# Performance work log

Measured on AMD Instinct MI355X. Metric: run time of the kernel, lower is better.

The kernel has to match this reference:

```python
import jax, jax.numpy as jnp
import numpy as np

NUM_ITER = 10  # torch forward default num_iter=10


def _normalize_rows(x):
    # x / (||x||_2 per row + 1e-6), matching torch data.norm(dim=1)[:, None]
    return x / (jnp.linalg.norm(x, axis=1, keepdims=True) + 1e-6)


def _cluster(data, init, cluster_temp, num_iter):
    # Soft k-means: normalize data once, then iterate
    # mu-normalize -> cosine sim -> softmax assignments -> weighted mean update.
    data = _normalize_rows(data)           # [N, D]
    mu = init                              # [K, D]
    dist = None
    for _ in range(num_iter):
        mu_n = _normalize_rows(mu)         # [K, D]
        dist = data @ mu_n.T               # [N, K]
        r = jax.nn.softmax(cluster_temp * dist, axis=1)  # [N, K]
        # diag(1/r.sum(0)) @ (r.T @ data) == row-wise divide
        mu = (r.T @ data) / r.sum(axis=0)[:, None]       # [K, D]
    r = jax.nn.softmax(cluster_temp * dist, axis=1)
    return mu, r


def setup_inputs() -> dict:
    key = jax.random.key(0)
    k1, k2 = jax.random.split(key)
    N, D, K = 100000, 512, 256
    embeds = jax.random.normal(k1, (N, D), dtype=jnp.float32)
    # self.init = torch.rand(K, nout): uniform [0, 1)
    init = jax.random.uniform(k2, (K, D), dtype=jnp.float32)
    cluster_temp = jnp.float32(30.0)
    return {"embeds": embeds, "cluster_temp": cluster_temp, "init": init}


def reference(embeds, cluster_temp, init):
    # First pass: 10 iterations from random init; result is detached in torch.
    mu_init, _ = _cluster(embeds, init, cluster_temp, NUM_ITER)
    mu_init = jax.lax.stop_gradient(mu_init)
    # Second pass: single iteration from detached means (grad flows here).
    mu, r = _cluster(embeds, mu_init, cluster_temp, 1)
    return mu, r
```

## Files before the change

### kernel.cpp

```cpp
#include <hip/hip_runtime.h>
#include <math.h>


#define DIMD 512
#define KCL 256
#define NSPLIT 96

typedef __attribute__((ext_vector_type(8))) short short8;
typedef __attribute__((ext_vector_type(4))) short short4v;
typedef __attribute__((ext_vector_type(4))) float float4v;

__device__ __forceinline__ short f2bf(float x) {
  union { float f; unsigned u; } v; v.f = x;
  unsigned r = v.u + 0x7fff + ((v.u >> 16) & 1);
  return (short)(r >> 16);
}
__device__ __forceinline__ float bf2f(short b) {
  union { unsigned u; float f; } v;
  v.u = ((unsigned)(unsigned short)b) << 16;
  return v.f;
}

__global__ void row_norms_k(const float* __restrict__ x,
                            float* __restrict__ inv_norm, int n) {
  int wave = threadIdx.x >> 6;
  int lane = threadIdx.x & 63;
  int row = blockIdx.x * 4 + wave;
  if (row >= n) return;
  const float4* xr = (const float4*)(x + (size_t)row * DIMD);
  float4 a = xr[lane];
  float4 b = xr[lane + 64];
  float s = a.x*a.x + a.y*a.y + a.z*a.z + a.w*a.w
          + b.x*b.x + b.y*b.y + b.z*b.z + b.w*b.w;
#pragma unroll
  for (int m = 32; m >= 1; m >>= 1) s += __shfl_xor(s, m);
  if (lane == 0) inv_norm[row] = 1.0f / (sqrtf(s) + 1e-6f);
}

__global__ void mu_norm_k(const float* __restrict__ mu_src,
                          const float* __restrict__ colsum_in,
                          short* __restrict__ mu_hi, short* __restrict__ mu_lo,
                          float* __restrict__ mu_acc_z,
                          float* __restrict__ colsum_z, int use_colsum) {
  int k = blockIdx.x;
  int t = threadIdx.x;
  float inv_c = 1.0f;
  if (use_colsum) inv_c = 1.0f / colsum_in[k];
  float v0 = mu_src[k * DIMD + t] * inv_c;
  float v1 = mu_src[k * DIMD + t + 256] * inv_c;
  float s = v0 * v0 + v1 * v1;
#pragma unroll
  for (int m = 32; m >= 1; m >>= 1) s += __shfl_xor(s, m);
  __shared__ float sred[4];
  int lane = t & 63, wv = t >> 6;
  if (lane == 0) sred[wv] = s;
  __syncthreads();
  s = sred[0] + sred[1] + sred[2] + sred[3];
  float inv = 1.0f / (sqrtf(s) + 1e-6f);
  float w0 = v0 * inv, w1 = v1 * inv;
  short h0 = f2bf(w0), h1 = f2bf(w1);
  mu_hi[k * DIMD + t] = h0;
  mu_hi[k * DIMD + t + 256] = h1;
  mu_lo[k * DIMD + t] = f2bf(w0 - bf2f(h0));
  mu_lo[k * DIMD + t + 256] = f2bf(w1 - bf2f(h1));
  mu_acc_z[k * DIMD + t] = 0.0f;
  mu_acc_z[k * DIMD + t + 256] = 0.0f;
  if (t == 0) colsum_z[k] = 0.0f;
}

__global__ void final_mu_k(const float* __restrict__ mu_acc,
                           const float* __restrict__ colsum,
                           float* __restrict__ out) {
  int k = blockIdx.x;
  int t = threadIdx.x;
  float ic = 1.0f / colsum[k];
  out[k * DIMD + t] = mu_acc[k * DIMD + t] * ic;
  out[k * DIMD + t + 256] = mu_acc[k * DIMD + t + 256] * ic;
}

__global__ __launch_bounds__(256) void dist_mfma_k(
    const float* __restrict__ data, const float* __restrict__ inv_norm,
    const short* __restrict__ mu_hi, const short* __restrict__ mu_lo,
    unsigned* __restrict__ r_pack, float* __restrict__ r_f32, int write_f32,
    float* __restrict__ colsum, const float* __restrict__ temp_p, int n) {
  __shared__ __align__(16) short a_lds[64][72];
  __shared__ __align__(16) short b_lds[256][72];
  __shared__ __align__(16) float red[64][4];

  int t = threadIdx.x;
  int wave = t >> 6, lane = t & 63, q = lane >> 4, lx = lane & 15;
  int i0 = blockIdx.x * 64;

  float4v acc[4][4];
#pragma unroll
  for (int mt = 0; mt < 4; ++mt)
#pragma unroll
    for (int nt = 0; nt < 4; ++nt) acc[mt][nt] = (float4v)0.0f;

  for (int ch = 0; ch < 16; ++ch) {
    int d0 = ch * 32;
    {
      int row = t >> 2, seg = t & 3;
      int gi = i0 + row;
      if (gi > n - 1) gi = n - 1;
      const float* p = data + (size_t)gi * DIMD + d0 + seg * 8;
      float4 x0 = *(const float4*)p;
      float4 x1 = *(const float4*)(p + 4);
      float sc = inv_norm[gi];
      float vv[8] = {x0.x * sc, x0.y * sc, x0.z * sc, x0.w * sc,
                     x1.x * sc, x1.y * sc, x1.z * sc, x1.w * sc};
      short8 hv, lv;
#pragma unroll
      for (int j = 0; j < 8; ++j) {
        short h = f2bf(vv[j]);
        hv[j] = h;
        lv[j] = f2bf(vv[j] - bf2f(h));
      }
      *(short8*)&a_lds[row][seg * 8] = hv;
      *(short8*)&a_lds[row][32 + seg * 8] = lv;
    }
    {
      int seg = t & 3, kb = t >> 2;
#pragma unroll
      for (int rep = 0; rep < 4; ++rep) {
        int k = rep * 64 + kb;
        short8 h = *(const short8*)(mu_hi + (size_t)k * DIMD + d0 + seg * 8);
        short8 l = *(const short8*)(mu_lo + (size_t)k * DIMD + d0 + seg * 8);
        *(short8*)&b_lds[k][seg * 8] = h;
        *(short8*)&b_lds[k][32 + seg * 8] = l;
      }
    }
    __syncthreads();
    short8 ah[4], al[4], bh[4], bl[4];
#pragma unroll
    for (int mt = 0; mt < 4; ++mt) {
      ah[mt] = *(const short8*)&a_lds[mt * 16 + lx][q * 8];
      al[mt] = *(const short8*)&a_lds[mt * 16 + lx][32 + q * 8];
    }
#pragma unroll
    for (int nt = 0; nt < 4; ++nt) {
      int kr = wave * 64 + nt * 16 + lx;
      bh[nt] = *(const short8*)&b_lds[kr][q * 8];
      bl[nt] = *(const short8*)&b_lds[kr][32 + q * 8];
    }
#pragma unroll
    for (int mt = 0; mt < 4; ++mt)
#pragma unroll
      for (int nt = 0; nt < 4; ++nt) {
        acc[mt][nt] = __builtin_amdgcn_mfma_f32_16x16x32_bf16(
            ah[mt], bh[nt], acc[mt][nt], 0, 0, 0);
        acc[mt][nt] = __builtin_amdgcn_mfma_f32_16x16x32_bf16(
            ah[mt], bl[nt], acc[mt][nt], 0, 0, 0);
        acc[mt][nt] = __builtin_amdgcn_mfma_f32_16x16x32_bf16(
            al[mt], bh[nt], acc[mt][nt], 0, 0, 0);
      }
    __syncthreads();
  }

  float tempv = temp_p[0];
  float rs[4][4];
#pragma unroll
  for (int mt = 0; mt < 4; ++mt)
#pragma unroll
    for (int reg = 0; reg < 4; ++reg) {
      float s = 0.0f;
#pragma unroll
      for (int nt = 0; nt < 4; ++nt) {
        float e = __expf(tempv * acc[mt][nt][reg]);
        acc[mt][nt][reg] = e;
        s += e;
      }
      s += __shfl_xor(s, 1);
      s += __shfl_xor(s, 2);
      s += __shfl_xor(s, 4);
      s += __shfl_xor(s, 8);
      rs[mt][reg] = s;
    }
  if (lx == 0) {
#pragma unroll
    for (int mt = 0; mt < 4; ++mt)
#pragma unroll
      for (int reg = 0; reg < 4; ++reg)
        red[mt * 16 + q * 4 + reg][wave] = rs[mt][reg];
  }
  __syncthreads();

  float cs[4] = {0.0f, 0.0f, 0.0f, 0.0f};
#pragma unroll
  for (int mt = 0; mt < 4; ++mt)
#pragma unroll
    for (int reg = 0; reg < 4; ++reg) {
      int row = mt * 16 + q * 4 + reg;
      float4 v = *(const float4*)&red[row][0];
      float is = 1.0f / (v.x + v.y + v.z + v.w);
      int gi = i0 + row;
      bool ok = gi < n;
#pragma unroll
      for (int nt = 0; nt < 4; ++nt) {
        float r = acc[mt][nt][reg] * is;
        acc[mt][nt][reg] = r;
        if (ok) cs[nt] += r;
      }
      if (ok) {
        if (write_f32) {
#pragma unroll
          for (int nt = 0; nt < 4; ++nt)
            r_f32[(size_t)gi * KCL + wave * 64 + nt * 16 + lx] =
                acc[mt][nt][reg];
        } else {
#pragma unroll
          for (int nt = 0; nt < 4; ++nt) {
            float r = acc[mt][nt][reg];
            short h = f2bf(r);
            short l = f2bf(r - bf2f(h));
            r_pack[(size_t)gi * KCL + wave * 64 + nt * 16 + lx] =
                ((unsigned)(unsigned short)h << 16) | (unsigned short)l;
          }
        }
      }
    }
#pragma unroll
  for (int nt = 0; nt < 4; ++nt) {
    cs[nt] += __shfl_xor(cs[nt], 16);
    cs[nt] += __shfl_xor(cs[nt], 32);
  }
  if (q == 0) {
#pragma unroll
    for (int nt = 0; nt < 4; ++nt)
      atomicAdd(&colsum[wave * 64 + nt * 16 + lx], cs[nt]);
  }
}

__global__ __launch_bounds__(256) void update_mfma_k(
    const unsigned* __restrict__ r_src, int r_is_f32,
    const float* __restrict__ data, const float* __restrict__ inv_norm,
    float* __restrict__ mu_acc, int n) {
  __shared__ __align__(16) short rT[128][72];
  __shared__ __align__(16) short xT[128][72];

  int t = threadIdx.x, wave = t >> 6, lane = t & 63, q = lane >> 4,
      lx = lane & 15;
  int bx = blockIdx.x;
  int k0 = (bx & 1) * 128, d0 = (bx >> 1) * 128;
  int ns = blockIdx.y;
  int chunk = (n + NSPLIT - 1) / NSPLIT;
  int ibeg = ns * chunk;
  int iend = ibeg + chunk;
  if (iend > n) iend = n;
  int wk = wave >> 1, wd = wave & 1;
  int iq = t >> 5, kq = t & 31;

  float4v acc[4][4];
#pragma unroll
  for (int mt = 0; mt < 4; ++mt)
#pragma unroll
    for (int nt = 0; nt < 4; ++nt) acc[mt][nt] = (float4v)0.0f;

  for (int ib = ibeg; ib < iend; ib += 32) {
    {
      short h[4][4], l[4][4];
#pragma unroll
      for (int ii = 0; ii < 4; ++ii) {
        int gi = ib + iq * 4 + ii;
        uint4 u = make_uint4(0u, 0u, 0u, 0u);
        if (gi < iend)
          u = *(const uint4*)(r_src + (size_t)gi * KCL + k0 + kq * 4);
        unsigned uu[4] = {u.x, u.y, u.z, u.w};
        if (r_is_f32) {
#pragma unroll
          for (int kk = 0; kk < 4; ++kk) {
            union { unsigned u; float f; } c; c.u = uu[kk];
            short hh = f2bf(c.f);
            h[ii][kk] = hh;
            l[ii][kk] = f2bf(c.f - bf2f(hh));
          }
        } else {
#pragma unroll
          for (int kk = 0; kk < 4; ++kk) {
            h[ii][kk] = (short)(uu[kk] >> 16);
            l[ii][kk] = (short)(uu[kk] & 0xffffu);
          }
        }
      }
#pragma unroll
      for (int kk = 0; kk < 4; ++kk) {
        short4v vh = {h[0][kk], h[1][kk], h[2][kk], h[3][kk]};
        short4v vl = {l[0][kk], l[1][kk], l[2][kk], l[3][kk]};
        *(short4v*)&rT[kq * 4 + kk][iq * 4] = vh;
        *(short4v*)&rT[kq * 4 + kk][32 + iq * 4] = vl;
      }
    }
    {
      short h[4][4], l[4][4];
#pragma unroll
      for (int ii = 0; ii < 4; ++ii) {
        int gi = ib + iq * 4 + ii;
        float4 x = make_float4(0.f, 0.f, 0.f, 0.f);
        float sc = 0.0f;
        if (gi < iend) {
          x = *(const float4*)(data + (size_t)gi * DIMD + d0 + kq * 4);
          sc = inv_norm[gi];
        }
        float vv[4] = {x.x * sc, x.y * sc, x.z * sc, x.w * sc};
#pragma unroll
        for (int kk = 0; kk < 4; ++kk) {
          short hh = f2bf(vv[kk]);
          h[ii][kk] = hh;
          l[ii][kk] = f2bf(vv[kk] - bf2f(hh));
        }
      }
#pragma unroll
      for (int kk = 0; kk < 4; ++kk) {
        short4v vh = {h[0][kk], h[1][kk], h[2][kk], h[3][kk]};
        short4v vl = {l[0][kk], l[1][kk], l[2][kk], l[3][kk]};
        *(short4v*)&xT[kq * 4 + kk][iq * 4] = vh;
        *(short4v*)&xT[kq * 4 + kk][32 + iq * 4] = vl;
      }
    }
    __syncthreads();
    short8 ah[4], al[4], bh[4], bl[4];
#pragma unroll
    for (int mt = 0; mt < 4; ++mt) {
      int kr = wk * 64 + mt * 16 + lx;
      ah[mt] = *(const short8*)&rT[kr][q * 8];
      al[mt] = *(const short8*)&rT[kr][32 + q * 8];
    }
#pragma unroll
    for (int nt = 0; nt < 4; ++nt) {
      int dr = wd * 64 + nt * 16 + lx;
      bh[nt] = *(const short8*)&xT[dr][q * 8];
      bl[nt] = *(const short8*)&xT[dr][32 + q * 8];
    }
#pragma unroll
    for (int mt = 0; mt < 4; ++mt)
#pragma unroll
      for (int nt = 0; nt < 4; ++nt) {
        acc[mt][nt] = __builtin_amdgcn_mfma_f32_16x16x32_bf16(
            ah[mt], bh[nt], acc[mt][nt], 0, 0, 0);
        acc[mt][nt] = __builtin_amdgcn_mfma_f32_16x16x32_bf16(
            ah[mt], bl[nt], acc[mt][nt], 0, 0, 0);
        acc[mt][nt] = __builtin_amdgcn_mfma_f32_16x16x32_bf16(
            al[mt], bh[nt], acc[mt][nt], 0, 0, 0);
      }
    __syncthreads();
  }
#pragma unroll
  for (int mt = 0; mt < 4; ++mt)
#pragma unroll
    for (int nt = 0; nt < 4; ++nt)
#pragma unroll
      for (int reg = 0; reg < 4; ++reg) {
        int k = k0 + wk * 64 + mt * 16 + q * 4 + reg;
        int d = d0 + wd * 64 + nt * 16 + lx;
        atomicAdd(&mu_acc[(size_t)k * DIMD + d], acc[mt][nt][reg]);
      }
}

extern "C" void kernel_launch(void* const* d_in, const int* in_sizes, int n_in,
                              void* d_out, int out_size, void* d_ws,
                              size_t ws_size, hipStream_t stream) {
  const float* embeds = (const float*)d_in[0];
  const float* temp_p = (const float*)d_in[1];
  const float* init = (const float*)d_in[2];
  int n = in_sizes[0] / DIMD;

  float* out_mu = (float*)d_out;
  float* out_r = (float*)d_out + KCL * DIMD;

  float* wsf = (float*)d_ws;
  float* inv_norm = wsf;
  float* mu_acc = wsf + ((n + 3) & ~3);
  float* colsum = mu_acc + KCL * DIMD;
  short* mu_hi = (short*)(colsum + 256);
  short* mu_lo = mu_hi + KCL * DIMD;

  row_norms_k<<<(n + 3) / 4, 256, 0, stream>>>(embeds, inv_norm, n);
  mu_norm_k<<<KCL, 256, 0, stream>>>(init, colsum, mu_hi, mu_lo, mu_acc,
                                     colsum, 0);

  for (int it = 0; it <= 10; ++it) {
    int wf32 = (it == 10) ? 1 : 0;
    dist_mfma_k<<<(n + 63) / 64, 256, 0, stream>>>(
        embeds, inv_norm, mu_hi, mu_lo, (unsigned*)out_r, out_r, wf32, colsum,
        temp_p, n);
    update_mfma_k<<<dim3(8, NSPLIT), 256, 0, stream>>>(
        (const unsigned*)out_r, wf32, embeds, inv_norm, mu_acc, n);
    if (it < 10) {
      mu_norm_k<<<KCL, 256, 0, stream>>>(mu_acc, colsum, mu_hi, mu_lo, mu_acc,
                                         colsum, 1);
    } else {
      final_mu_k<<<KCL, 256, 0, stream>>>(mu_acc, colsum, out_mu);
    }
  }
}
```

Baseline: 3.878 ms.

## Store assignments transposed, read mu directly from global, swizzle packed LDS tiles

```diff
diff --git a/kernel.cpp b/kernel.cpp
--- a/kernel.cpp
+++ b/kernel.cpp
@@ -5,26 +5,38 @@
 #define DIMD 512
 #define KCL 256
 #define NSPLIT 96
+#define SWZ(r) ((((r) >> 3) ^ (r)) & 7)
 
 typedef __attribute__((ext_vector_type(8))) short short8;
-typedef __attribute__((ext_vector_type(4))) short short4v;
 typedef __attribute__((ext_vector_type(4))) float float4v;
 
-__device__ __forceinline__ short f2bf(float x) {
+__device__ __forceinline__ unsigned f2bf_u(float x) {
   union { float f; unsigned u; } v; v.f = x;
-  unsigned r = v.u + 0x7fff + ((v.u >> 16) & 1);
-  return (short)(r >> 16);
-}
-__device__ __forceinline__ float bf2f(short b) {
-  union { unsigned u; float f; } v;
-  v.u = ((unsigned)(unsigned short)b) << 16;
-  return v.f;
+  return (v.u + 0x7fff + ((v.u >> 16) & 1)) >> 16;
+}
+__device__ __forceinline__ float bf2f_u(unsigned b) {
+  union { unsigned u; float f; } v; v.u = b << 16; return v.f;
+}
+__device__ __forceinline__ unsigned packhl(float x) {
+  unsigned h = f2bf_u(x);
+  unsigned l = f2bf_u(x - bf2f_u(h));
+  return (h << 16) | l;
+}
+__device__ __forceinline__ void unpack8(const unsigned* u, short8& hi,
+                                        short8& lo) {
+  union { unsigned w[4]; short8 s; } H, L;
+#pragma unroll
+  for (int p = 0; p < 4; ++p) {
+    unsigned a = u[2 * p], b = u[2 * p + 1];
+    H.w[p] = (a >> 16) | (b & 0xffff0000u);
+    L.w[p] = (a & 0xffffu) | (b << 16);
+  }
+  hi = H.s; lo = L.s;
 }
 
 __global__ void row_norms_k(const float* __restrict__ x,
                             float* __restrict__ inv_norm, int n) {
-  int wave = threadIdx.x >> 6;
-  int lane = threadIdx.x & 63;
+  int wave = threadIdx.x >> 6, lane = threadIdx.x & 63;
   int row = blockIdx.x * 4 + wave;
   if (row >= n) return;
   const float4* xr = (const float4*)(x + (size_t)row * DIMD);
@@ -42,10 +54,8 @@
                           short* __restrict__ mu_hi, short* __restrict__ mu_lo,
                           float* __restrict__ mu_acc_z,
                           float* __restrict__ colsum_z, int use_colsum) {
-  int k = blockIdx.x;
-  int t = threadIdx.x;
-  float inv_c = 1.0f;
-  if (use_colsum) inv_c = 1.0f / colsum_in[k];
+  int k = blockIdx.x, t = threadIdx.x;
+  float inv_c = use_colsum ? 1.0f / colsum_in[k] : 1.0f;
   float v0 = mu_src[k * DIMD + t] * inv_c;
   float v1 = mu_src[k * DIMD + t + 256] * inv_c;
   float s = v0 * v0 + v1 * v1;
@@ -58,11 +68,11 @@
   s = sred[0] + sred[1] + sred[2] + sred[3];
   float inv = 1.0f / (sqrtf(s) + 1e-6f);
   float w0 = v0 * inv, w1 = v1 * inv;
-  short h0 = f2bf(w0), h1 = f2bf(w1);
-  mu_hi[k * DIMD + t] = h0;
-  mu_hi[k * DIMD + t + 256] = h1;
-  mu_lo[k * DIMD + t] = f2bf(w0 - bf2f(h0));
-  mu_lo[k * DIMD + t + 256] = f2bf(w1 - bf2f(h1));
+  unsigned h0 = f2bf_u(w0), h1 = f2bf_u(w1);
+  mu_hi[k * DIMD + t] = (short)h0;
+  mu_hi[k * DIMD + t + 256] = (short)h1;
+  mu_lo[k * DIMD + t] = (short)f2bf_u(w0 - bf2f_u(h0));
+  mu_lo[k * DIMD + t + 256] = (short)f2bf_u(w1 - bf2f_u(h1));
   mu_acc_z[k * DIMD + t] = 0.0f;
   mu_acc_z[k * DIMD + t + 256] = 0.0f;
   if (t == 0) colsum_z[k] = 0.0f;
@@ -71,8 +81,7 @@
 __global__ void final_mu_k(const float* __restrict__ mu_acc,
                            const float* __restrict__ colsum,
                            float* __restrict__ out) {
-  int k = blockIdx.x;
-  int t = threadIdx.x;
+  int k = blockIdx.x, t = threadIdx.x;
   float ic = 1.0f / colsum[k];
   out[k * DIMD + t] = mu_acc[k * DIMD + t] * ic;
   out[k * DIMD + t + 256] = mu_acc[k * DIMD + t + 256] * ic;
@@ -81,15 +90,21 @@
 __global__ __launch_bounds__(256) void dist_mfma_k(
     const float* __restrict__ data, const float* __restrict__ inv_norm,
     const short* __restrict__ mu_hi, const short* __restrict__ mu_lo,
-    unsigned* __restrict__ r_pack, float* __restrict__ r_f32, int write_f32,
+    unsigned* __restrict__ rT, float* __restrict__ r_f32, int write_f32,
     float* __restrict__ colsum, const float* __restrict__ temp_p, int n) {
-  __shared__ __align__(16) short a_lds[64][72];
-  __shared__ __align__(16) short b_lds[256][72];
-  __shared__ __align__(16) float red[64][4];
-
-  int t = threadIdx.x;
-  int wave = t >> 6, lane = t & 63, q = lane >> 4, lx = lane & 15;
+  __shared__ unsigned a_lds[64][32];
+  __shared__ float red[64][4];
+
+  int t = threadIdx.x, wave = t >> 6, lane = t & 63, q = lane >> 4,
+      lx = lane & 15;
   int i0 = blockIdx.x * 64;
+  int arow = t >> 3, achk = t & 7;
+  int gi0 = min(i0 + arow, n - 1), gi1 = min(i0 + arow + 32, n - 1);
+  float sc0 = inv_norm[gi0], sc1 = inv_norm[gi1];
+  const float* p0 = data + (size_t)gi0 * DIMD + achk * 4;
+  const float* p1 = data + (size_t)gi1 * DIMD + achk * 4;
+  int c0 = (achk ^ SWZ(arow)) * 4;
+  int c1 = (achk ^ SWZ(arow + 32)) * 4;
 
   float4v acc[4][4];
 #pragma unroll
@@ -99,49 +114,31 @@
 
   for (int ch = 0; ch < 16; ++ch) {
     int d0 = ch * 32;
-    {
-      int row = t >> 2, seg = t & 3;
-      int gi = i0 + row;
-      if (gi > n - 1) gi = n - 1;
-      const float* p = data + (size_t)gi * DIMD + d0 + seg * 8;
-      float4 x0 = *(const float4*)p;
-      float4 x1 = *(const float4*)(p + 4);
-      float sc = inv_norm[gi];
-      float vv[8] = {x0.x * sc, x0.y * sc, x0.z * sc, x0.w * sc,
-                     x1.x * sc, x1.y * sc, x1.z * sc, x1.w * sc};
-      short8 hv, lv;
-#pragma unroll
-      for (int j = 0; j < 8; ++j) {
-        short h = f2bf(vv[j]);
-        hv[j] = h;
-        lv[j] = f2bf(vv[j] - bf2f(h));
-      }
-      *(short8*)&a_lds[row][seg * 8] = hv;
-      *(short8*)&a_lds[row][32 + seg * 8] = lv;
-    }
-    {
-      int seg = t & 3, kb = t >> 2;
-#pragma unroll
-      for (int rep = 0; rep < 4; ++rep) {
-        int k = rep * 64 + kb;
-        short8 h = *(const short8*)(mu_hi + (size_t)k * DIMD + d0 + seg * 8);
-        short8 l = *(const short8*)(mu_lo + (size_t)k * DIMD + d0 + seg * 8);
-        *(short8*)&b_lds[k][seg * 8] = h;
-        *(short8*)&b_lds[k][32 + seg * 8] = l;
-      }
-    }
+    float4 v0 = *(const float4*)(p0 + d0);
+    float4 v1 = *(const float4*)(p1 + d0);
+    uint4 u0, u1;
+    u0.x = packhl(v0.x * sc0); u0.y = packhl(v0.y * sc0);
+    u0.z = packhl(v0.z * sc0); u0.w = packhl(v0.w * sc0);
+    u1.x = packhl(v1.x * sc1); u1.y = packhl(v1.y * sc1);
+    u1.z = packhl(v1.z * sc1); u1.w = packhl(v1.w * sc1);
+    *(uint4*)&a_lds[arow][c0] = u0;
+    *(uint4*)&a_lds[arow + 32][c1] = u1;
     __syncthreads();
+
     short8 ah[4], al[4], bh[4], bl[4];
 #pragma unroll
     for (int mt = 0; mt < 4; ++mt) {
-      ah[mt] = *(const short8*)&a_lds[mt * 16 + lx][q * 8];
-      al[mt] = *(const short8*)&a_lds[mt * 16 + lx][32 + q * 8];
+      int row = mt * 16 + lx, s = SWZ(row);
+      unsigned u[8];
+      *(uint4*)&u[0] = *(const uint4*)&a_lds[row][((2 * q) ^ s) * 4];
+      *(uint4*)&u[4] = *(const uint4*)&a_lds[row][((2 * q + 1) ^ s) * 4];
+      unpack8(u, ah[mt], al[mt]);
     }
 #pragma unroll
     for (int nt = 0; nt < 4; ++nt) {
       int kr = wave * 64 + nt * 16 + lx;
-      bh[nt] = *(const short8*)&b_lds[kr][q * 8];
-      bl[nt] = *(const short8*)&b_lds[kr][32 + q * 8];
+      bh[nt] = *(const short8*)(mu_hi + (size_t)kr * DIMD + d0 + q * 8);
+      bl[nt] = *(const short8*)(mu_lo + (size_t)kr * DIMD + d0 + q * 8);
     }
 #pragma unroll
     for (int mt = 0; mt < 4; ++mt)
@@ -201,24 +198,36 @@
         acc[mt][nt][reg] = r;
         if (ok) cs[nt] += r;
       }
-      if (ok) {
-        if (write_f32) {
+    }
+  if (!write_f32) {
+#pragma unroll
+    for (int mt = 0; mt < 4; ++mt) {
+      int ibase = i0 + mt * 16 + q * 4;
+      if (ibase < n) {
+#pragma unroll
+        for (int nt = 0; nt < 4; ++nt) {
+          int k = wave * 64 + nt * 16 + lx;
+          uint4 u;
+          u.x = packhl(acc[mt][nt][0]); u.y = packhl(acc[mt][nt][1]);
+          u.z = packhl(acc[mt][nt][2]); u.w = packhl(acc[mt][nt][3]);
+          *(uint4*)(rT + (size_t)k * n + ibase) = u;
+        }
+      }
+    }
+  } else {
+#pragma unroll
+    for (int mt = 0; mt < 4; ++mt)
+#pragma unroll
+      for (int reg = 0; reg < 4; ++reg) {
+        int gi = i0 + mt * 16 + q * 4 + reg;
+        if (gi < n) {
 #pragma unroll
           for (int nt = 0; nt < 4; ++nt)
             r_f32[(size_t)gi * KCL + wave * 64 + nt * 16 + lx] =
                 acc[mt][nt][reg];
-        } else {
-#pragma unroll
-          for (int nt = 0; nt < 4; ++nt) {
-            float r = acc[mt][nt][reg];
-            short h = f2bf(r);
-            short l = f2bf(r - bf2f(h));
-            r_pack[(size_t)gi * KCL + wave * 64 + nt * 16 + lx] =
-                ((unsigned)(unsigned short)h << 16) | (unsigned short)l;
-          }
         }
       }
-    }
+  }
 #pragma unroll
   for (int nt = 0; nt < 4; ++nt) {
     cs[nt] += __shfl_xor(cs[nt], 16);
@@ -232,23 +241,21 @@
 }
 
 __global__ __launch_bounds__(256) void update_mfma_k(
-    const unsigned* __restrict__ r_src, int r_is_f32,
-    const float* __restrict__ data, const float* __restrict__ inv_norm,
-    float* __restrict__ mu_acc, int n) {
-  __shared__ __align__(16) short rT[128][72];
-  __shared__ __align__(16) short xT[128][72];
+    const unsigned* __restrict__ rT, const float* __restrict__ r_f32,
+    int r_is_f32, const float* __restrict__ data,
+    const float* __restrict__ inv_norm, float* __restrict__ mu_acc, int n) {
+  __shared__ unsigned xT[128][32];
+  __shared__ unsigned rL[128][32];
 
   int t = threadIdx.x, wave = t >> 6, lane = t & 63, q = lane >> 4,
       lx = lane & 15;
   int bx = blockIdx.x;
   int k0 = (bx & 1) * 128, d0 = (bx >> 1) * 128;
-  int ns = blockIdx.y;
   int chunk = (n + NSPLIT - 1) / NSPLIT;
-  int ibeg = ns * chunk;
-  int iend = ibeg + chunk;
-  if (iend > n) iend = n;
+  int ibeg = blockIdx.y * chunk;
+  int iend = min(ibeg + chunk, n);
   int wk = wave >> 1, wd = wave & 1;
-  int iq = t >> 5, kq = t & 31;
+  int dq = t & 31, iq4 = t >> 5;
 
   float4v acc[4][4];
 #pragma unroll
@@ -257,79 +264,83 @@
     for (int nt = 0; nt < 4; ++nt) acc[mt][nt] = (float4v)0.0f;
 
   for (int ib = ibeg; ib < iend; ib += 32) {
+    int rem = iend - ib;
     {
-      short h[4][4], l[4][4];
+      float4 xv[4];
 #pragma unroll
       for (int ii = 0; ii < 4; ++ii) {
-        int gi = ib + iq * 4 + ii;
-        uint4 u = make_uint4(0u, 0u, 0u, 0u);
-        if (gi < iend)
-          u = *(const uint4*)(r_src + (size_t)gi * KCL + k0 + kq * 4);
-        unsigned uu[4] = {u.x, u.y, u.z, u.w};
-        if (r_is_f32) {
-#pragma unroll
-          for (int kk = 0; kk < 4; ++kk) {
-            union { unsigned u; float f; } c; c.u = uu[kk];
-            short hh = f2bf(c.f);
-            h[ii][kk] = hh;
-            l[ii][kk] = f2bf(c.f - bf2f(hh));
-          }
+        int gi = ib + iq4 * 4 + ii;
+        if (gi < iend) {
+          float4 v = *(const float4*)(data + (size_t)gi * DIMD + d0 + dq * 4);
+          float sc = inv_norm[gi];
+          v.x *= sc; v.y *= sc; v.z *= sc; v.w *= sc;
+          xv[ii] = v;
+        } else
+          xv[ii] = make_float4(0.f, 0.f, 0.f, 0.f);
+      }
+#pragma unroll
+      for (int r = 0; r < 4; ++r) {
+        int d = dq * 4 + r;
+        uint4 u;
+        u.x = packhl((&xv[0].x)[r]); u.y = packhl((&xv[1].x)[r]);
+        u.z = packhl((&xv[2].x)[r]); u.w = packhl((&xv[3].x)[r]);
+        *(uint4*)&xT[d][(iq4 ^ SWZ(d)) * 4] = u;
+      }
+    }
+    if (r_is_f32) {
+      float4 rv[4];
+#pragma unroll
+      for (int ii = 0; ii < 4; ++ii) {
+        int gi = ib + iq4 * 4 + ii;
+        rv[ii] = (gi < iend)
+                     ? *(const float4*)(r_f32 + (size_t)gi * KCL + k0 + dq * 4)
+                     : make_float4(0.f, 0.f, 0.f, 0.f);
+      }
+#pragma unroll
+      for (int r = 0; r < 4; ++r) {
+        int k = dq * 4 + r;
+        uint4 u;
+        u.x = packhl((&rv[0].x)[r]); u.y = packhl((&rv[1].x)[r]);
+        u.z = packhl((&rv[2].x)[r]); u.w = packhl((&rv[3].x)[r]);
+        *(uint4*)&rL[k][(iq4 ^ SWZ(k)) * 4] = u;
+      }
+    }
+    short8 ah[4], al[4];
+    if (!r_is_f32) {
+#pragma unroll
+      for (int mt = 0; mt < 4; ++mt) {
+        int kr = k0 + wk * 64 + mt * 16 + lx;
+        const unsigned* p = rT + (size_t)kr * n + ib + q * 8;
+        unsigned u[8];
+        if (rem >= 32) {
+          *(uint4*)&u[0] = *(const uint4*)p;
+          *(uint4*)&u[4] = *(const uint4*)(p + 4);
         } else {
 #pragma unroll
-          for (int kk = 0; kk < 4; ++kk) {
-            h[ii][kk] = (short)(uu[kk] >> 16);
-            l[ii][kk] = (short)(uu[kk] & 0xffffu);
-          }
+          for (int j = 0; j < 8; ++j) u[j] = (q * 8 + j < rem) ? p[j] : 0u;
         }
-      }
-#pragma unroll
-      for (int kk = 0; kk < 4; ++kk) {
-        short4v vh = {h[0][kk], h[1][kk], h[2][kk], h[3][kk]};
-        short4v vl = {l[0][kk], l[1][kk], l[2][kk], l[3][kk]};
-        *(short4v*)&rT[kq * 4 + kk][iq * 4] = vh;
-        *(short4v*)&rT[kq * 4 + kk][32 + iq * 4] = vl;
-      }
-    }
-    {
-      short h[4][4], l[4][4];
-#pragma unroll
-      for (int ii = 0; ii < 4; ++ii) {
-        int gi = ib + iq * 4 + ii;
-        float4 x = make_float4(0.f, 0.f, 0.f, 0.f);
-        float sc = 0.0f;
-        if (gi < iend) {
-          x = *(const float4*)(data + (size_t)gi * DIMD + d0 + kq * 4);
-          sc = inv_norm[gi];
-        }
-        float vv[4] = {x.x * sc, x.y * sc, x.z * sc, x.w * sc};
-#pragma unroll
-        for (int kk = 0; kk < 4; ++kk) {
-          short hh = f2bf(vv[kk]);
-          h[ii][kk] = hh;
-          l[ii][kk] = f2bf(vv[kk] - bf2f(hh));
-        }
-      }
-#pragma unroll
-      for (int kk = 0; kk < 4; ++kk) {
-        short4v vh = {h[0][kk], h[1][kk], h[2][kk], h[3][kk]};
-        short4v vl = {l[0][kk], l[1][kk], l[2][kk], l[3][kk]};
-        *(short4v*)&xT[kq * 4 + kk][iq * 4] = vh;
-        *(short4v*)&xT[kq * 4 + kk][32 + iq * 4] = vl;
+        unpack8(u, ah[mt], al[mt]);
       }
     }
     __syncthreads();
-    short8 ah[4], al[4], bh[4], bl[4];
-#pragma unroll
-    for (int mt = 0; mt < 4; ++mt) {
-      int kr = wk * 64 + mt * 16 + lx;
-      ah[mt] = *(const short8*)&rT[kr][q * 8];
-      al[mt] = *(const short8*)&rT[kr][32 + q * 8];
-    }
+    if (r_is_f32) {
+#pragma unroll
+      for (int mt = 0; mt < 4; ++mt) {
+        int kl = wk * 64 + mt * 16 + lx, s = SWZ(kl);
+        unsigned u[8];
+        *(uint4*)&u[0] = *(const uint4*)&rL[kl][((2 * q) ^ s) * 4];
+        *(uint4*)&u[4] = *(const uint4*)&rL[kl][((2 * q + 1) ^ s) * 4];
+        unpack8(u, ah[mt], al[mt]);
+      }
+    }
+    short8 bh[4], bl[4];
 #pragma unroll
     for (int nt = 0; nt < 4; ++nt) {
-      int dr = wd * 64 + nt * 16 + lx;
-      bh[nt] = *(const short8*)&xT[dr][q * 8];
-      bl[nt] = *(const short8*)&xT[dr][32 + q * 8];
+      int dl = wd * 64 + nt * 16 + lx, s = SWZ(dl);
+      unsigned u[8];
+      *(uint4*)&u[0] = *(const uint4*)&xT[dl][((2 * q) ^ s) * 4];
+      *(uint4*)&u[4] = *(const uint4*)&xT[dl][((2 * q + 1) ^ s) * 4];
+      unpack8(u, bh[nt], bl[nt]);
     }
 #pragma unroll
     for (int mt = 0; mt < 4; ++mt)
@@ -384,7 +395,7 @@
         embeds, inv_norm, mu_hi, mu_lo, (unsigned*)out_r, out_r, wf32, colsum,
         temp_p, n);
     update_mfma_k<<<dim3(8, NSPLIT), 256, 0, stream>>>(
-        (const unsigned*)out_r, wf32, embeds, inv_norm, mu_acc, n);
+        (const unsigned*)out_r, out_r, wf32, embeds, inv_norm, mu_acc, n);
     if (it < 10) {
       mu_norm_k<<<KCL, 256, 0, stream>>>(mu_acc, colsum, mu_hi, mu_lo, mu_acc,
                                          colsum, 1);
```

Result: slower. 6.075 ms (+56.6%).
